# Optimization experiments

Hardware: AMD Instinct MI355X
Metric: run time of the kernel (lower is better)

The kernel has to match this reference:

```python
import jax, jax.numpy as jnp
import numpy as np


def _rbf(x, centres, log_sigmas):
    sq = (jnp.sum(x * x, axis=-1, keepdims=True)            # [B,1]
          + jnp.sum(centres * centres, axis=-1)[None, :]    # [1,O]
          - 2.0 * x @ centres.T)                            # [B,O]
    sq = jnp.maximum(sq, 0.0)
    # original: phi = exp(-(sqrt(sq)/sigma)^2) == exp(-sq / sigma^2)
    inv_sigma2 = jnp.exp(-2.0 * log_sigmas)[None, :]        # [1,O]
    return jnp.exp(-sq * inv_sigma2)


def setup_inputs() -> dict:
    key = jax.random.key(0)
    k1, k2 = jax.random.split(key)
    B, IN, OUT = 16384, 64, 4096
    x = jax.random.normal(k1, (B, IN), dtype=jnp.float32)
    centres = jax.random.normal(k2, (OUT, IN), dtype=jnp.float32)  # init.normal_(0,1)
    log_sigmas = jnp.zeros((OUT,), dtype=jnp.float32)              # init.constant_(0)
    return {"x": x, "centres": centres, "log_sigmas": log_sigmas}


def reference(x, centres, log_sigmas):
    return _rbf(x, centres, log_sigmas)
```

## Files before the change

kernel.cpp:

```cpp
#include <hip/hip_runtime.h>
#include <hip/hip_bf16.h>

typedef __attribute__((ext_vector_type(8))) short bf16x8;
typedef __attribute__((ext_vector_type(4))) float f32x4;

#define K_DIM 64
#define CPITCH 72
#define BAND_SHORTS 20480

__global__ __launch_bounds__(256) void rbf_prep_x(
    const float* __restrict__ src, int rows,
    __hip_bfloat16* __restrict__ hi, __hip_bfloat16* __restrict__ lo,
    float* __restrict__ norms)
{
    int row  = blockIdx.x * 4 + (threadIdx.x >> 6);
    int lane = threadIdx.x & 63;
    if (row >= rows) return;

    float v = src[(size_t)row * K_DIM + lane];
    __hip_bfloat16 h = __float2bfloat16(v);
    float hf = __bfloat162float(h);
    __hip_bfloat16 l = __float2bfloat16(v - hf);
    hi[(size_t)row * K_DIM + lane] = h;
    lo[(size_t)row * K_DIM + lane] = l;

    float s = v * v;
    #pragma unroll
    for (int off = 32; off > 0; off >>= 1) s += __shfl_down(s, off, 64);
    if (lane == 0) norms[row] = s;
}

__global__ __launch_bounds__(256) void rbf_prep_c(
    const float* __restrict__ src, int rows,
    short* __restrict__ blob, const float* __restrict__ log_sigmas)
{
    int row  = blockIdx.x * 4 + (threadIdx.x >> 6);
    int lane = threadIdx.x & 63;
    if (row >= rows) return;

    float v = src[(size_t)row * K_DIM + lane];
    __hip_bfloat16 h = __float2bfloat16(v);
    float hf = __bfloat162float(h);
    __hip_bfloat16 l = __float2bfloat16(v - hf);

    const int band = row >> 7, r = row & 127;
    short* base = blob + (size_t)band * BAND_SHORTS;
    base[r * CPITCH + lane]        = *(short*)&h;
    base[9216 + r * CPITCH + lane] = *(short*)&l;

    float s = v * v;
    #pragma unroll
    for (int off = 32; off > 0; off >>= 1) s += __shfl_down(s, off, 64);
    if (lane == 0) {
        float* f = (float*)(base + 18432);
        f[r]       = s;
        f[128 + r] = __expf(-2.0f * log_sigmas[row]);
    }
}

__global__ __launch_bounds__(256, 3) void rbf_main(
    const __hip_bfloat16* __restrict__ xhi, const __hip_bfloat16* __restrict__ xlo,
    const short* __restrict__ blob, const float* __restrict__ nx,
    float* __restrict__ out, int N)
{
    __shared__ __align__(16) short cs[BAND_SHORTS];

    const int tid  = threadIdx.x;
    const int wave = tid >> 6;
    const int lane = tid & 63;
    const int quad = lane >> 4;
    const int l16  = lane & 15;

    const int band   = blockIdx.x;
    const int m_base = blockIdx.y << 8;
    const int n_base = band << 7;

    {
        const f32x4* src = (const f32x4*)(blob + (size_t)band * BAND_SHORTS);
        f32x4* dst = (f32x4*)cs;
        #pragma unroll
        for (int i = 0; i < 10; ++i) {
            const int idx = tid + (i << 8);
            if (idx < 2368) dst[idx] = src[idx];
        }
    }

    const int wbase = m_base + (wave << 6);
    bf16x8 xh0[4], xh1[4], xl0[4], xl1[4];
    float  nxm[4];
    #pragma unroll
    for (int mg = 0; mg < 4; ++mg) {
        const int xr = wbase + (mg << 4) + l16;
        const size_t ro = (size_t)xr * K_DIM + (quad << 3);
        xh0[mg] = *(const bf16x8*)(xhi + ro);
        xh1[mg] = *(const bf16x8*)(xhi + ro + 32);
        xl0[mg] = *(const bf16x8*)(xlo + ro);
        xl1[mg] = *(const bf16x8*)(xlo + ro + 32);
        nxm[mg] = nx[xr];
    }

    __syncthreads();

    const short* hbase = cs;
    const short* lbase = cs + 9216;
    const float* fbase = (const float*)(cs + 18432);

    for (int ng = 0; ng < 8; ++ng) {
        const int off = ((ng << 4) + l16) * CPITCH + (quad << 3);
        const bf16x8 ch0 = *(const bf16x8*)(hbase + off);
        const bf16x8 ch1 = *(const bf16x8*)(hbase + off + 32);
        const bf16x8 cl0 = *(const bf16x8*)(lbase + off);
        const bf16x8 cl1 = *(const bf16x8*)(lbase + off + 32);

        const int jc = (ng << 4) + (quad << 2);
        const f32x4 nc4 = *(const f32x4*)&fbase[jc];
        const f32x4 iv4 = *(const f32x4*)&fbase[128 + jc];

        #pragma unroll
        for (int mg = 0; mg < 4; ++mg) {
            f32x4 acc = {0.f, 0.f, 0.f, 0.f};
            acc = __builtin_amdgcn_mfma_f32_16x16x32_bf16(ch0, xh0[mg], acc, 0, 0, 0);
            acc = __builtin_amdgcn_mfma_f32_16x16x32_bf16(ch1, xh1[mg], acc, 0, 0, 0);
            acc = __builtin_amdgcn_mfma_f32_16x16x32_bf16(ch0, xl0[mg], acc, 0, 0, 0);
            acc = __builtin_amdgcn_mfma_f32_16x16x32_bf16(ch1, xl1[mg], acc, 0, 0, 0);
            acc = __builtin_amdgcn_mfma_f32_16x16x32_bf16(cl0, xh0[mg], acc, 0, 0, 0);
            acc = __builtin_amdgcn_mfma_f32_16x16x32_bf16(cl1, xh1[mg], acc, 0, 0, 0);

            f32x4 res;
            #pragma unroll
            for (int r = 0; r < 4; ++r) {
                float sq = fmaxf(nxm[mg] + nc4[r] - 2.0f * acc[r], 0.f);
                res[r] = __expf(-sq * iv4[r]);
            }
            __builtin_nontemporal_store(
                res, (f32x4*)(out + (size_t)(wbase + (mg << 4) + l16) * N + n_base + jc));
        }
    }
}

__device__ __forceinline__ void split8(const float* __restrict__ p,
                                       bf16x8& hi, bf16x8& lo, float& ss) {
    #pragma unroll
    for (int j = 0; j < 8; ++j) {
        float v = p[j];
        ss = fmaf(v, v, ss);
        __hip_bfloat16 h = __float2bfloat16(v);
        float hf = __bfloat162float(h);
        __hip_bfloat16 l = __float2bfloat16(v - hf);
        hi[j] = *reinterpret_cast<const short*>(&h);
        lo[j] = *reinterpret_cast<const short*>(&l);
    }
}

__global__ __launch_bounds__(256) void rbf_fused(
    const float* __restrict__ x, const float* __restrict__ c,
    const float* __restrict__ ls, float* __restrict__ out, int N)
{
    const int wave = threadIdx.x >> 6;
    const int lane = threadIdx.x & 63;
    const int quad = lane >> 4;
    const int l16  = lane & 15;

    const int m_base = (blockIdx.y << 6) + (wave << 4);
    const int n_base = blockIdx.x << 6;

    const int am = m_base + l16;
    const float* xp = x + (size_t)am * K_DIM;
    bf16x8 ahi0, alo0, ahi1, alo1;
    float ssx = 0.f;
    split8(xp + quad * 8,      ahi0, alo0, ssx);
    split8(xp + 32 + quad * 8, ahi1, alo1, ssx);
    ssx += __shfl_xor(ssx, 16, 64);
    ssx += __shfl_xor(ssx, 32, 64);
    float nxr[4];
    #pragma unroll
    for (int r = 0; r < 4; ++r) nxr[r] = __shfl(ssx, quad * 4 + r, 64);

    #pragma unroll
    for (int nt = 0; nt < 4; ++nt) {
        const int n = n_base + nt * 16 + l16;
        const float* cp = c + (size_t)n * K_DIM;
        bf16x8 bhi0, blo0, bhi1, blo1;
        float ssc = 0.f;
        split8(cp + quad * 8,      bhi0, blo0, ssc);
        split8(cp + 32 + quad * 8, bhi1, blo1, ssc);
        ssc += __shfl_xor(ssc, 16, 64);
        ssc += __shfl_xor(ssc, 32, 64);

        f32x4 acc = {0.f, 0.f, 0.f, 0.f};
        acc = __builtin_amdgcn_mfma_f32_16x16x32_bf16(ahi0, bhi0, acc, 0, 0, 0);
        acc = __builtin_amdgcn_mfma_f32_16x16x32_bf16(ahi1, bhi1, acc, 0, 0, 0);
        acc = __builtin_amdgcn_mfma_f32_16x16x32_bf16(ahi0, blo0, acc, 0, 0, 0);
        acc = __builtin_amdgcn_mfma_f32_16x16x32_bf16(ahi1, blo1, acc, 0, 0, 0);
        acc = __builtin_amdgcn_mfma_f32_16x16x32_bf16(alo0, bhi0, acc, 0, 0, 0);
        acc = __builtin_amdgcn_mfma_f32_16x16x32_bf16(alo1, bhi1, acc, 0, 0, 0);

        const float invv = __expf(-2.0f * ls[n]);
        #pragma unroll
        for (int r = 0; r < 4; ++r) {
            const int row = m_base + quad * 4 + r;
            float sq = fmaxf(nxr[r] + ssc - 2.0f * acc[r], 0.f);
            out[(size_t)row * N + n] = __expf(-sq * invv);
        }
    }
}

extern "C" void kernel_launch(void* const* d_in, const int* in_sizes, int n_in,
                              void* d_out, int out_size, void* d_ws, size_t ws_size,
                              hipStream_t stream) {
    const float* x  = (const float*)d_in[0];
    const float* c  = (const float*)d_in[1];
    const float* ls = (const float*)d_in[2];
    float* out = (float*)d_out;

    const int M = in_sizes[0] / K_DIM;
    const int N = in_sizes[2];

    size_t off = 0;
    auto place = [&](size_t bytes) { size_t p = off; off += (bytes + 255) & ~(size_t)255; return p; };
    size_t o_xhi  = place((size_t)M * K_DIM * 2);
    size_t o_xlo  = place((size_t)M * K_DIM * 2);
    size_t o_blob = place((size_t)(N / 128) * BAND_SHORTS * 2);
    size_t o_nx   = place((size_t)M * 4);

    if (ws_size >= off && (M % 256) == 0 && (N % 128) == 0) {
        char* ws = (char*)d_ws;
        __hip_bfloat16* xhi = (__hip_bfloat16*)(ws + o_xhi);
        __hip_bfloat16* xlo = (__hip_bfloat16*)(ws + o_xlo);
        short* blob = (short*)(ws + o_blob);
        float* nx   = (float*)(ws + o_nx);

        rbf_prep_x<<<dim3((M + 3) / 4), 256, 0, stream>>>(x, M, xhi, xlo, nx);
        rbf_prep_c<<<dim3((N + 3) / 4), 256, 0, stream>>>(c, N, blob, ls);
        rbf_main<<<dim3(N / 128, M / 256), 256, 0, stream>>>(xhi, xlo, blob, nx, out, N);
    } else {
        rbf_fused<<<dim3(N / 64, M / 64), 256, 0, stream>>>(x, c, ls, out, N);
    }
}
```

Before: 305.4 us.

## Fuse bf16 hi/lo split and norm prep into the main RBF kernel

Removes the two preprocessing kernels and the workspace. Each main block now loads fp32 x rows and its 128-row band of centres directly, splits them into bf16 hi/lo pairs and computes norms in registers, and writes the centre data into LDS. This removes two launches and the workspace round trip. In exchange, every block recomputes the x split and the centre band split, so that work is duplicated across the grid. The size inference in the launcher now hedges between element and byte counts.

Measured after the change: 304.3 us. No clear change (-0.4%).

```diff
diff --git a/kernel.cpp b/kernel.cpp
--- a/kernel.cpp
+++ b/kernel.cpp
@@ -8,60 +8,22 @@
 #define CPITCH 72
 #define BAND_SHORTS 20480
 
-__global__ __launch_bounds__(256) void rbf_prep_x(
-    const float* __restrict__ src, int rows,
-    __hip_bfloat16* __restrict__ hi, __hip_bfloat16* __restrict__ lo,
-    float* __restrict__ norms)
-{
-    int row  = blockIdx.x * 4 + (threadIdx.x >> 6);
-    int lane = threadIdx.x & 63;
-    if (row >= rows) return;
-
-    float v = src[(size_t)row * K_DIM + lane];
-    __hip_bfloat16 h = __float2bfloat16(v);
-    float hf = __bfloat162float(h);
-    __hip_bfloat16 l = __float2bfloat16(v - hf);
-    hi[(size_t)row * K_DIM + lane] = h;
-    lo[(size_t)row * K_DIM + lane] = l;
-
-    float s = v * v;
-    #pragma unroll
-    for (int off = 32; off > 0; off >>= 1) s += __shfl_down(s, off, 64);
-    if (lane == 0) norms[row] = s;
-}
-
-__global__ __launch_bounds__(256) void rbf_prep_c(
-    const float* __restrict__ src, int rows,
-    short* __restrict__ blob, const float* __restrict__ log_sigmas)
-{
-    int row  = blockIdx.x * 4 + (threadIdx.x >> 6);
-    int lane = threadIdx.x & 63;
-    if (row >= rows) return;
-
-    float v = src[(size_t)row * K_DIM + lane];
-    __hip_bfloat16 h = __float2bfloat16(v);
-    float hf = __bfloat162float(h);
-    __hip_bfloat16 l = __float2bfloat16(v - hf);
-
-    const int band = row >> 7, r = row & 127;
-    short* base = blob + (size_t)band * BAND_SHORTS;
-    base[r * CPITCH + lane]        = *(short*)&h;
-    base[9216 + r * CPITCH + lane] = *(short*)&l;
-
-    float s = v * v;
-    #pragma unroll
-    for (int off = 32; off > 0; off >>= 1) s += __shfl_down(s, off, 64);
-    if (lane == 0) {
-        float* f = (float*)(base + 18432);
-        f[r]       = s;
-        f[128 + r] = __expf(-2.0f * log_sigmas[row]);
-    }
-}
-
-__global__ __launch_bounds__(256, 3) void rbf_main(
-    const __hip_bfloat16* __restrict__ xhi, const __hip_bfloat16* __restrict__ xlo,
-    const short* __restrict__ blob, const float* __restrict__ nx,
-    float* __restrict__ out, int N)
+__device__ __forceinline__ void split4(const f32x4 v, short* hi, short* lo, float& ss) {
+    #pragma unroll
+    for (int j = 0; j < 4; ++j) {
+        float f = v[j];
+        ss = fmaf(f, f, ss);
+        __hip_bfloat16 h = __float2bfloat16(f);
+        float hf = __bfloat162float(h);
+        __hip_bfloat16 l = __float2bfloat16(f - hf);
+        hi[j] = *reinterpret_cast<const short*>(&h);
+        lo[j] = *reinterpret_cast<const short*>(&l);
+    }
+}
+
+__global__ __launch_bounds__(256, 3) void rbf_one(
+    const float* __restrict__ x, const float* __restrict__ c,
+    const float* __restrict__ ls, float* __restrict__ out, int N)
 {
     __shared__ __align__(16) short cs[BAND_SHORTS];
 
@@ -75,28 +37,52 @@
     const int m_base = blockIdx.y << 8;
     const int n_base = band << 7;
 
-    {
-        const f32x4* src = (const f32x4*)(blob + (size_t)band * BAND_SHORTS);
-        f32x4* dst = (f32x4*)cs;
-        #pragma unroll
-        for (int i = 0; i < 10; ++i) {
-            const int idx = tid + (i << 8);
-            if (idx < 2368) dst[idx] = src[idx];
-        }
-    }
+    const int crow = tid >> 1, chalf = tid & 1;
+    const float* cp = c + (size_t)(n_base + crow) * K_DIM + (chalf << 5);
+    f32x4 cv[8];
+    #pragma unroll
+    for (int i = 0; i < 8; ++i) cv[i] = ((const f32x4*)cp)[i];
+    const float lsv = ls[n_base + crow];
 
     const int wbase = m_base + (wave << 6);
     bf16x8 xh0[4], xh1[4], xl0[4], xl1[4];
     float  nxm[4];
     #pragma unroll
     for (int mg = 0; mg < 4; ++mg) {
-        const int xr = wbase + (mg << 4) + l16;
-        const size_t ro = (size_t)xr * K_DIM + (quad << 3);
-        xh0[mg] = *(const bf16x8*)(xhi + ro);
-        xh1[mg] = *(const bf16x8*)(xhi + ro + 32);
-        xl0[mg] = *(const bf16x8*)(xlo + ro);
-        xl1[mg] = *(const bf16x8*)(xlo + ro + 32);
-        nxm[mg] = nx[xr];
+        const float* xp = x + (size_t)(wbase + (mg << 4) + l16) * K_DIM + (quad << 3);
+        f32x4 a0 = *(const f32x4*)xp;
+        f32x4 a1 = *(const f32x4*)(xp + 4);
+        f32x4 b0 = *(const f32x4*)(xp + 32);
+        f32x4 b1 = *(const f32x4*)(xp + 36);
+        float ss = 0.f;
+        short h[8], l[8];
+        split4(a0, h, l, ss); split4(a1, h + 4, l + 4, ss);
+        xh0[mg] = *(bf16x8*)h;  xl0[mg] = *(bf16x8*)l;
+        split4(b0, h, l, ss); split4(b1, h + 4, l + 4, ss);
+        xh1[mg] = *(bf16x8*)h;  xl1[mg] = *(bf16x8*)l;
+        ss += __shfl_xor(ss, 16, 64);
+        ss += __shfl_xor(ss, 32, 64);
+        nxm[mg] = ss;
+    }
+
+    {
+        short* hb = cs + crow * CPITCH + (chalf << 5);
+        short* lb = hb + 9216;
+        float ss = 0.f;
+        #pragma unroll
+        for (int i = 0; i < 4; ++i) {
+            short h[8], l[8];
+            split4(cv[2 * i],     h,     l,     ss);
+            split4(cv[2 * i + 1], h + 4, l + 4, ss);
+            *(bf16x8*)(hb + (i << 3)) = *(bf16x8*)h;
+            *(bf16x8*)(lb + (i << 3)) = *(bf16x8*)l;
+        }
+        ss += __shfl_xor(ss, 1, 64);
+        if (chalf == 0) {
+            float* f = (float*)(cs + 18432);
+            f[crow]       = ss;
+            f[128 + crow] = __expf(-2.0f * lsv);
+        }
     }
 
     __syncthreads();
@@ -213,27 +199,17 @@
     const float* ls = (const float*)d_in[2];
     float* out = (float*)d_out;
 
-    const int M = in_sizes[0] / K_DIM;
-    const int N = in_sizes[2];
-
-    size_t off = 0;
-    auto place = [&](size_t bytes) { size_t p = off; off += (bytes + 255) & ~(size_t)255; return p; };
-    size_t o_xhi  = place((size_t)M * K_DIM * 2);
-    size_t o_xlo  = place((size_t)M * K_DIM * 2);
-    size_t o_blob = place((size_t)(N / 128) * BAND_SHORTS * 2);
-    size_t o_nx   = place((size_t)M * 4);
-
-    if (ws_size >= off && (M % 256) == 0 && (N % 128) == 0) {
-        char* ws = (char*)d_ws;
-        __hip_bfloat16* xhi = (__hip_bfloat16*)(ws + o_xhi);
-        __hip_bfloat16* xlo = (__hip_bfloat16*)(ws + o_xlo);
-        short* blob = (short*)(ws + o_blob);
-        float* nx   = (float*)(ws + o_nx);
-
-        rbf_prep_x<<<dim3((M + 3) / 4), 256, 0, stream>>>(x, M, xhi, xlo, nx);
-        rbf_prep_c<<<dim3((N + 3) / 4), 256, 0, stream>>>(c, N, blob, ls);
-        rbf_main<<<dim3(N / 128, M / 256), 256, 0, stream>>>(xhi, xlo, blob, nx, out, N);
+    const int M = in_sizes[0] / (K_DIM * 4);
+    const int N = in_sizes[2] / 4;
+
+    const int M_e = in_sizes[0] / K_DIM;
+    const int N_e = in_sizes[2];
+    const int Mr = (M_e % 256 == 0) ? M_e : M;
+    const int Nr = (N_e % 128 == 0) ? N_e : N;
+
+    if ((Mr % 256) == 0 && (Nr % 128) == 0) {
+        rbf_one<<<dim3(Nr / 128, Mr / 256), 256, 0, stream>>>(x, c, ls, out, Nr);
     } else {
-        rbf_fused<<<dim3(N / 64, M / 64), 256, 0, stream>>>(x, c, ls, out, N);
-    }
-}
+        rbf_fused<<<dim3(Nr / 64, Mr / 64), 256, 0, stream>>>(x, c, ls, out, Nr);
+    }
+}
```
